# Kernel tuning notes

Measured on AMD Instinct MI355X. Metric: run time of the kernel, lower is better.

## Reference

```python
import jax, jax.numpy as jnp
import numpy as np

N_HEADS, N_LEVELS, N_POINTS = 8, 4, 4
D_MODEL, RNN, ENC, ATT_HID = 512, 512, 512, 512
D_HEAD = D_MODEL // N_HEADS  # att_feat_size = clip_context_dim / cap_nheads = 64
B = 1024
LEVEL_LENS = [1024, 512, 256, 128]
T_TOTAL = sum(LEVEL_LENS)


def setup_inputs() -> dict:
    key = jax.random.key(0)
    ks = jax.random.split(key, 24)
    s = 0.02  # weight init scale
    inp = {
        'xt': jax.random.normal(ks[0], (B, ENC), jnp.float32),
        'h0': jax.random.normal(ks[1], (2, B, RNN), jnp.float32),
        'c0': jax.random.normal(ks[2], (2, B, RNN), jnp.float32),
        'query': jax.random.normal(ks[3], (1, B, D_MODEL), jnp.float32),
        'reference_points': jax.random.uniform(ks[4], (1, B, N_LEVELS, 1), jnp.float32),
        'input_flatten': jax.random.normal(ks[5], (1, T_TOTAL, D_MODEL), jnp.float32),
        'input_spatial_shapes': jnp.asarray(LEVEL_LENS, jnp.int32),
        'input_level_start_index': jnp.asarray(np.cumsum([0] + LEVEL_LENS[:-1]), jnp.int32),
        'input_padding_mask': jnp.zeros((1, T_TOTAL), jnp.bool_),
        # MSDeformAttnCap params (query side sees cat(h, query) -> 2*D_MODEL)
        'W_value': jax.random.normal(ks[6], (D_MODEL, D_MODEL), jnp.float32) * s,
        'b_value': jnp.zeros((D_MODEL,), jnp.float32),
        'W_off': jax.random.normal(ks[7], (2 * D_MODEL, N_HEADS * N_LEVELS * N_POINTS), jnp.float32) * s,
        'b_off': jax.random.normal(ks[8], (N_HEADS * N_LEVELS * N_POINTS,), jnp.float32) * s,
        'W_attw': jax.random.normal(ks[9], (2 * D_MODEL, N_HEADS * N_LEVELS * N_POINTS), jnp.float32) * s,
        'b_attw': jnp.zeros((N_HEADS * N_LEVELS * N_POINTS,), jnp.float32),
        # additive SAT attention
        'W_ctx': jax.random.normal(ks[10], (D_HEAD, ATT_HID), jnp.float32) * s,
        'b_ctx': jnp.zeros((ATT_HID,), jnp.float32),
        'W_h2a': jax.random.normal(ks[11], (RNN, ATT_HID), jnp.float32) * s,
        'b_h2a': jnp.zeros((ATT_HID,), jnp.float32),
        'w_alpha': jax.random.normal(ks[12], (ATT_HID, 1), jnp.float32) * s,
        'b_alpha': jnp.zeros((1,), jnp.float32),
        # 2-layer LSTM, bias=False; input = ENC + 2*D_MODEL = 1536
        'Wih0': jax.random.normal(ks[13], (4 * RNN, ENC + 2 * D_MODEL), jnp.float32) * s,
        'Whh0': jax.random.normal(ks[14], (4 * RNN, RNN), jnp.float32) * s,
        'Wih1': jax.random.normal(ks[15], (4 * RNN, RNN), jnp.float32) * s,
        'Whh1': jax.random.normal(ks[16], (4 * RNN, RNN), jnp.float32) * s,
    }
    return inp


def _lstm_cell(x, h, c, Wih, Whh):
    g = x @ Wih.T + h @ Whh.T
    i, f, gg, o = jnp.split(g, 4, axis=-1)
    c2 = jax.nn.sigmoid(f) * c + jax.nn.sigmoid(i) * jnp.tanh(gg)
    h2 = jax.nn.sigmoid(o) * jnp.tanh(c2)
    return h2, c2


def reference(xt, h0, c0, query, reference_points, input_flatten,
              input_spatial_shapes, input_level_start_index, input_padding_mask,
              W_value, b_value, W_off, b_off, W_attw, b_attw,
              W_ctx, b_ctx, W_h2a, b_h2a, w_alpha, b_alpha,
              Wih0, Whh0, Wih1, Whh1):
    h_last = h0[-1]                                            # (B, RNN)
    jq = jnp.concatenate([h_last, query[0]], axis=-1)          # (B, 2D) joint query

    # ---- MSDeformAttnCap: value proj + 1D multi-level point sampling ----
    v = input_flatten[0] @ W_value + b_value                   # (T, D)
    v = jnp.where(input_padding_mask[0][:, None], 0.0, v)
    v = v.reshape(-1, N_HEADS, D_HEAD).transpose(1, 0, 2)     # (H, T, Dh)

    off = (jq @ W_off + b_off).reshape(B, N_HEADS, N_LEVELS, N_POINTS)
    aw = (jq @ W_attw + b_attw).reshape(B, N_HEADS, N_LEVELS * N_POINTS)
    aw = jax.nn.softmax(aw, axis=-1).reshape(B, N_HEADS, N_LEVELS, N_POINTS)

    Tf = input_spatial_shapes.astype(jnp.float32)              # (L,)
    ref = reference_points[0, :, :, 0]                          # (B, L) normalized centers
    loc = ref[:, None, :, None] + off / Tf[None, None, :, None]  # (B,H,L,P) in [0,1]

    # grid_sample(align_corners=False, zeros padding) linear interp along T
    x = loc * Tf[None, None, :, None] - 0.5
    x0 = jnp.floor(x)
    w1 = x - x0
    Ti = input_spatial_shapes[None, None, :, None]
    x0i = x0.astype(jnp.int32)
    valid0 = ((x0i >= 0) & (x0i < Ti)).astype(v.dtype)
    valid1 = ((x0i + 1 >= 0) & (x0i + 1 < Ti)).astype(v.dtype)
    start = input_level_start_index[None, None, :, None]
    i0 = jnp.clip(x0i, 0, Ti - 1) + start
    i1 = jnp.clip(x0i + 1, 0, Ti - 1) + start
    hids = jnp.arange(N_HEADS)[None, :, None, None]
    v0 = v[hids, i0]                                            # (B,H,L,P,Dh)
    v1 = v[hids, i1]
    samp = v0 * ((1.0 - w1) * valid0)[..., None] + v1 * (w1 * valid1)[..., None]
    # weighted sampled values, NOT summed over points (Cap variant)
    clip_feats = (samp * aw[..., None]).reshape(B, N_HEADS, N_LEVELS * N_POINTS, D_HEAD)

    # ---- additive SAT attention over the L*P sampled slots ----
    att_h = h_last @ W_h2a + b_h2a                              # (B, A)
    att = jnp.tanh(clip_feats @ W_ctx + b_ctx + att_h[:, None, None, :])  # (B,H,LP,A)
    dot = (att @ w_alpha)[..., 0] + b_alpha[0]                  # (B,H,LP)
    w = jax.nn.softmax(dot, axis=-1)
    att_res = jnp.einsum('bhp,bhpd->bhd', w, clip_feats).reshape(B, N_HEADS * D_HEAD)

    # ---- LSTM step (2 layers, bias=False, eval mode -> no dropout) ----
    x_in = jnp.concatenate([xt, att_res, query[0]], axis=-1)   # (B, ENC+2D)
    h1, c1 = _lstm_cell(x_in, h0[0], c0[0], Wih0, Whh0)
    h2, c2 = _lstm_cell(h1, h0[1], c0[1], Wih1, Whh1)
    h_new = jnp.stack([h1, h2])
    c_new = jnp.stack([c1, c2])
    return h2, h_new, c_new
```

## Files before the change

kernel.cpp:

```cpp
#include <hip/hip_runtime.h>
#include <math.h>


typedef __attribute__((ext_vector_type(8))) short          s16x8;
typedef __attribute__((ext_vector_type(8))) unsigned short u16x8;
typedef __attribute__((ext_vector_type(4))) float          f32x4;

#define LOG2E  1.4426950408889634f
#define LOG2E2 2.8853900817779268f

__device__ __forceinline__ float rcpf(float x) { return __builtin_amdgcn_rcpf(x); }
__device__ __forceinline__ float exp2f_fast(float x) { return __builtin_amdgcn_exp2f(x); }
__device__ __forceinline__ float sigf(float x) {
    return rcpf(1.0f + exp2f_fast(-x * LOG2E));
}
__device__ __forceinline__ float tanhf_fast(float x) {
    const float xc = fminf(fmaxf(x, -15.0f), 15.0f);
    const float e2 = exp2f_fast(xc * LOG2E2);
    return 1.0f - 2.0f * rcpf(e2 + 1.0f);
}
__device__ __forceinline__ unsigned short f2bf(float f) {
    unsigned u = __float_as_uint(f);
    u += 0x7FFF + ((u >> 16) & 1);
    return (unsigned short)(u >> 16);
}
__device__ __forceinline__ float bf2f(unsigned short h) {
    return __uint_as_float(((unsigned)h) << 16);
}
__device__ __forceinline__ void gld_lds16(const unsigned short* g, unsigned short* l) {
    __builtin_amdgcn_global_load_lds(
        (const __attribute__((address_space(1))) void*)g,
        (__attribute__((address_space(3))) void*)l, 16, 0, 0);
}

struct CvtJob { const float* src; unsigned short* dst; int sld, dld, cols, total, ilv; };
struct CvtJobs { CvtJob j[11]; };
__global__ __launch_bounds__(256) void cvt_bf16(CvtJobs cj) {
    const CvtJob jb = cj.j[blockIdx.y];
    const int i = (blockIdx.x * 256 + threadIdx.x) * 4;
    if (i >= jb.total) return;
    const int r = i / jb.cols, c = i - r * jb.cols;
    const int rd = jb.ilv ? (((r & 511) << 2) | (r >> 9)) : r;
    const float4 v4 = *(const float4*)&jb.src[(size_t)r * jb.sld + c];
    ushort4 o;
    o.x = f2bf(v4.x); o.y = f2bf(v4.y); o.z = f2bf(v4.z); o.w = f2bf(v4.w);
    *(ushort4*)&jb.dst[(size_t)rd * jb.dld + c] = o;
}

struct TJob { const float* src; unsigned short* dst; int N_, dld, K_, total; };
struct TJobs { TJob j[6]; };
__global__ __launch_bounds__(256) void tcvt_bf16(TJobs tj) {
    const TJob jb = tj.j[blockIdx.y];
    const int tilesN = jb.N_ >> 5, tilesK = jb.K_ >> 5;
    const int tile = blockIdx.x;
    if (tile >= tilesN * tilesK) return;
    const int tn0 = (tile % tilesN) << 5, tk0 = (tile / tilesN) << 5;
    __shared__ float lds[32][33];
    const int t = threadIdx.x;
    if (jb.src) {
#pragma unroll
        for (int q = 0; q < 4; ++q) {
            const int e = t + (q << 8);
            lds[e >> 5][e & 31] = jb.src[(size_t)(tk0 + (e >> 5)) * jb.N_ + tn0 + (e & 31)];
        }
        __syncthreads();
#pragma unroll
        for (int q = 0; q < 4; ++q) {
            const int e = t + (q << 8);
            const int n = e >> 5, k = e & 31;
            jb.dst[(size_t)(tn0 + n) * jb.dld + tk0 + k] = f2bf(lds[k][n]);
        }
    } else {
#pragma unroll
        for (int q = 0; q < 4; ++q) {
            const int e = t + (q << 8);
            jb.dst[(size_t)(tn0 + (e >> 5)) * jb.dld + tk0 + (e & 31)] = 0;
        }
    }
}

__global__ __launch_bounds__(768) void bias_cat3(const float* __restrict__ a,
                                                 const float* __restrict__ b,
                                                 const float* __restrict__ c,
                                                 float* __restrict__ dst) {
    const int t = threadIdx.x;
    dst[t] = (t < 128) ? a[t] : (t < 256 ? b[t - 128] : c[t - 256]);
}


#define STAGE_T(buf, k0) do { \
        gld_lds16(Ag1 + (k0), &As[buf][s1 * 8]); \
        gld_lds16(Ag2 + (k0), &As[buf][s2 * 8]); \
        gld_lds16(Bg1 + (k0), &Bs[buf][s1 * 8]); \
        gld_lds16(Bg2 + (k0), &Bs[buf][s2 * 8]); } while (0)

#define WAIT_INFL(t) do { \
        const int infl_ = nsteps - 1 - (t); \
        if (infl_ >= 2)      asm volatile("s_waitcnt vmcnt(8)" ::: "memory"); \
        else if (infl_ == 1) asm volatile("s_waitcnt vmcnt(4)" ::: "memory"); \
        else                 asm volatile("s_waitcnt vmcnt(0)" ::: "memory"); \
        __builtin_amdgcn_s_barrier(); } while (0)

__global__ __launch_bounds__(256) void sgemm(
    const unsigned short* __restrict__ A, int lda,
    const unsigned short* __restrict__ B, int ldb,
    const float* __restrict__ bias, float* __restrict__ C, int ldc, int K)
{
    __shared__ unsigned short As[4][64 * 64];
    __shared__ unsigned short Bs[4][64 * 64];

    const int tid = threadIdx.x;
    const int w = tid >> 6, lane = tid & 63;
    const int wr = w >> 1, wc = w & 1;
    const int lr = lane & 15, lg = lane >> 4;
    const int bm = blockIdx.y, bn = blockIdx.x;

    const int s1 = tid, s2 = tid + 256;
    const int r1 = s1 >> 3, c1 = ((s1 & 7) ^ (r1 & 7)) << 3;
    const int r2 = s2 >> 3, c2 = ((s2 & 7) ^ (r2 & 7)) << 3;
    const unsigned short* Ag1 = A + (size_t)(bm * 64 + r1) * lda + c1;
    const unsigned short* Ag2 = A + (size_t)(bm * 64 + r2) * lda + c2;
    const unsigned short* Bg1 = B + (size_t)(bn * 64 + r1) * ldb + c1;
    const unsigned short* Bg2 = B + (size_t)(bn * 64 + r2) * ldb + c2;

    f32x4 acc[2][2];
#pragma unroll
    for (int mt = 0; mt < 2; ++mt)
#pragma unroll
        for (int nt = 0; nt < 2; ++nt) acc[mt][nt] = (f32x4){0.f, 0.f, 0.f, 0.f};

    const int nsteps = K >> 6;
    STAGE_T(0, 0);
    if (nsteps > 1) STAGE_T(1, 64);
    if (nsteps > 2) STAGE_T(2, 128);

    for (int t = 0; t < nsteps; ++t) {
        WAIT_INFL(t);
        if (t + 3 < nsteps)
            STAGE_T((t + 3) & 3, (t + 3) << 6);
        const unsigned short* Ab = &As[t & 3][0];
        const unsigned short* Bb = &Bs[t & 3][0];
        s16x8 a[2][2], bfr[2][2];
#pragma unroll
        for (int mt = 0; mt < 2; ++mt) {
            const int ar = wr * 32 + mt * 16 + lr;
#pragma unroll
            for (int ks = 0; ks < 2; ++ks)
                a[mt][ks] = *(const s16x8*)&Ab[(ar * 8 + ((ks * 4 + lg) ^ (ar & 7))) * 8];
        }
#pragma unroll
        for (int nt = 0; nt < 2; ++nt) {
            const int br = wc * 32 + nt * 16 + lr;
#pragma unroll
            for (int ks = 0; ks < 2; ++ks)
                bfr[nt][ks] = *(const s16x8*)&Bb[(br * 8 + ((ks * 4 + lg) ^ (br & 7))) * 8];
        }
#pragma unroll
        for (int ks = 0; ks < 2; ++ks)
#pragma unroll
            for (int mt = 0; mt < 2; ++mt)
#pragma unroll
                for (int nt = 0; nt < 2; ++nt)
                    acc[mt][nt] = __builtin_amdgcn_mfma_f32_16x16x32_bf16(
                        a[mt][ks], bfr[nt][ks], acc[mt][nt], 0, 0, 0);
    }
#pragma unroll
    for (int nt = 0; nt < 2; ++nt) {
        const int col = bn * 64 + wc * 32 + nt * 16 + lr;
        const float bb = bias ? bias[col] : 0.0f;
#pragma unroll
        for (int mt = 0; mt < 2; ++mt) {
            const int rbase = bm * 64 + wr * 32 + mt * 16 + lg * 4;
#pragma unroll
            for (int r = 0; r < 4; ++r)
                C[(size_t)(rbase + r) * ldc + col] = acc[mt][nt][r] + bb;
        }
    }
}

__global__ __launch_bounds__(256) void sgemm_lstm(
    const unsigned short* __restrict__ A, int lda,
    const unsigned short* __restrict__ B, int ldb,
    const float* __restrict__ c_in,
    float* __restrict__ h_a, float* __restrict__ h_b,
    unsigned short* __restrict__ hbf, int hbf_ld,
    float* __restrict__ c_out, int K)
{
    __shared__ unsigned short As[4][64 * 64];
    __shared__ unsigned short Bs[4][64 * 64];

    const int tid = threadIdx.x;
    const int w = tid >> 6, lane = tid & 63;
    const int wr = w >> 1, wc = w & 1;
    const int lr = lane & 15, lg = lane >> 4;
    const int bm = blockIdx.y, bn = blockIdx.x;

    const int s1 = tid, s2 = tid + 256;
    const int r1 = s1 >> 3, c1 = ((s1 & 7) ^ (r1 & 7)) << 3;
    const int r2 = s2 >> 3, c2 = ((s2 & 7) ^ (r2 & 7)) << 3;
    const unsigned short* Ag1 = A + (size_t)(bm * 64 + r1) * lda + c1;
    const unsigned short* Ag2 = A + (size_t)(bm * 64 + r2) * lda + c2;
    const unsigned short* Bg1 = B + (size_t)(bn * 64 + r1) * ldb + c1;
    const unsigned short* Bg2 = B + (size_t)(bn * 64 + r2) * ldb + c2;

    f32x4 acc[2][2];
#pragma unroll
    for (int mt = 0; mt < 2; ++mt)
#pragma unroll
        for (int nt = 0; nt < 2; ++nt) acc[mt][nt] = (f32x4){0.f, 0.f, 0.f, 0.f};

    const int nsteps = K >> 6;
    STAGE_T(0, 0);
    if (nsteps > 1) STAGE_T(1, 64);
    if (nsteps > 2) STAGE_T(2, 128);

    for (int t = 0; t < nsteps; ++t) {
        WAIT_INFL(t);
        if (t + 3 < nsteps)
            STAGE_T((t + 3) & 3, (t + 3) << 6);
        const unsigned short* Ab = &As[t & 3][0];
        const unsigned short* Bb = &Bs[t & 3][0];
        s16x8 a[2][2], bfr[2][2];
#pragma unroll
        for (int mt = 0; mt < 2; ++mt) {
            const int ar = wr * 32 + mt * 16 + lr;
#pragma unroll
            for (int ks = 0; ks < 2; ++ks)
                a[mt][ks] = *(const s16x8*)&Ab[(ar * 8 + ((ks * 4 + lg) ^ (ar & 7))) * 8];
        }
#pragma unroll
        for (int nt = 0; nt < 2; ++nt) {
            const int br = wc * 32 + nt * 16 + lr;
#pragma unroll
            for (int ks = 0; ks < 2; ++ks)
                bfr[nt][ks] = *(const s16x8*)&Bb[(br * 8 + ((ks * 4 + lg) ^ (br & 7))) * 8];
        }
#pragma unroll
        for (int ks = 0; ks < 2; ++ks)
#pragma unroll
            for (int mt = 0; mt < 2; ++mt)
#pragma unroll
                for (int nt = 0; nt < 2; ++nt)
                    acc[mt][nt] = __builtin_amdgcn_mfma_f32_16x16x32_bf16(
                        a[mt][ks], bfr[nt][ks], acc[mt][nt], 0, 0, 0);
    }
    const int gte  = lane & 3;
    const int base = lane & ~3;
#pragma unroll
    for (int nt = 0; nt < 2; ++nt) {
        const int col = bn * 64 + wc * 32 + nt * 16 + lr;
        const int u = col >> 2;
#pragma unroll
        for (int mt = 0; mt < 2; ++mt) {
            const int rbase = bm * 64 + wr * 32 + mt * 16 + lg * 4;
#pragma unroll
            for (int r = 0; r < 4; ++r) {
                const float vv = acc[mt][nt][r];
                const float a  = (gte == 2) ? tanhf_fast(vv) : sigf(vv);
                const float ai = __shfl(a, base + 0);
                const float af = __shfl(a, base + 1);
                const float ag = __shfl(a, base + 2);
                const float ao = __shfl(a, base + 3);
                const int row = rbase + r;
                const float c  = c_in[(size_t)row * 512 + u];
                const float c2 = af * c + ai * ag;
                const float h2 = ao * tanhf_fast(c2);
                if (gte == 0)      c_out[(size_t)row * 512 + u] = c2;
                else if (gte == 1) h_a[(size_t)row * 512 + u] = h2;
                else if (gte == 2) { if (h_b) h_b[(size_t)row * 512 + u] = h2; }
                else if (hbf)      hbf[(size_t)row * hbf_ld + u] = f2bf(h2);
            }
        }
    }
}
#undef STAGE_T
#undef WAIT_INFL

__global__ __launch_bounds__(512, 2) void fused_att(
    const float* __restrict__ v,
    const float* __restrict__ obat,
    const float* __restrict__ refp,
    const int*   __restrict__ shapes,
    const int*   __restrict__ starts,
    const unsigned short* __restrict__ Wb,
    const float* __restrict__ bctx,
    const float* __restrict__ walpha,
    unsigned short* __restrict__ attdst)
{
    __shared__ unsigned short cf[128 * 64];
    __shared__ float ba[512];
    __shared__ float wal[512];
    __shared__ float awb[128];
    __shared__ float dsum[128];
    __shared__ float dots4[4][128];

    const int b   = blockIdx.x;
    const int tid = threadIdx.x;

    if (tid < 128) awb[tid] = obat[b * 768 + 128 + tid];
    __syncthreads();
    if (tid < 8) {
        float mx = -1e30f;
        for (int i = 0; i < 16; ++i) mx = fmaxf(mx, awb[tid * 16 + i]);
        float sum = 0.f;
        for (int i = 0; i < 16; ++i) { float e = exp2f_fast((awb[tid * 16 + i] - mx) * LOG2E); awb[tid * 16 + i] = e; sum += e; }
        float inv = rcpf(sum);
        for (int i = 0; i < 16; ++i) awb[tid * 16 + i] *= inv;
    }
    __syncthreads();

    ba[tid]  = bctx[tid] + obat[b * 768 + 256 + tid];
    wal[tid] = walpha[tid];
    {
        const int pg  = tid >> 2;
        const int sub = tid & 3;
        const int d0  = sub * 16;
        const int h   = pg >> 4;
        const int l   = (pg & 15) >> 2;
        const int Tlen = shapes[l];
        const int st   = starts[l];
        const float T  = (float)Tlen;
        const float refv = refp[b * 4 + l];
        const float offv = obat[b * 768 + pg];
        const float awv  = awb[pg];
        const float x   = (refv + offv * rcpf(T)) * T - 0.5f;
        const float x0f = floorf(x);
        const float w1  = x - x0f;
        const int   x0  = (int)x0f;
        const float w0s = (x0 >= 0 && x0 < Tlen) ? (1.0f - w1) : 0.0f;
        const float w1s = (x0 + 1 >= 0 && x0 + 1 < Tlen) ? w1 : 0.0f;
        const int i0 = (min(max(x0, 0), Tlen - 1) + st) * 512 + h * 64;
        const int i1 = (min(max(x0 + 1, 0), Tlen - 1) + st) * 512 + h * 64;
        u16x8 o0, o1;
#pragma unroll
        for (int q = 0; q < 4; ++q) {
            const float4 a  = *(const float4*)&v[i0 + d0 + q * 4];
            const float4 bq = *(const float4*)&v[i1 + d0 + q * 4];
            unsigned short e0 = f2bf((a.x * w0s + bq.x * w1s) * awv);
            unsigned short e1 = f2bf((a.y * w0s + bq.y * w1s) * awv);
            unsigned short e2 = f2bf((a.z * w0s + bq.z * w1s) * awv);
            unsigned short e3 = f2bf((a.w * w0s + bq.w * w1s) * awv);
            if (q == 0) { o0[0] = e0; o0[1] = e1; o0[2] = e2; o0[3] = e3; }
            if (q == 1) { o0[4] = e0; o0[5] = e1; o0[6] = e2; o0[7] = e3; }
            if (q == 2) { o1[0] = e0; o1[1] = e1; o1[2] = e2; o1[3] = e3; }
            if (q == 3) { o1[4] = e0; o1[5] = e1; o1[6] = e2; o1[7] = e3; }
        }
        const int c0 = (sub * 2)     ^ (pg & 7);
        const int c1 = (sub * 2 + 1) ^ (pg & 7);
        *(u16x8*)&cf[pg * 64 + c0 * 8] = o0;
        *(u16x8*)&cf[pg * 64 + c1 * 8] = o1;
    }
    __syncthreads();

    {
        const int w    = tid >> 6, lane = tid & 63;
        const int wm   = w >> 2, wn = w & 3;
        const int lr   = lane & 15, lg = lane >> 4;

        s16x8 afrag[4][2];
#pragma unroll
        for (int mt = 0; mt < 4; ++mt) {
            const int row = wm * 64 + mt * 16 + lr;
#pragma unroll
            for (int ks = 0; ks < 2; ++ks) {
                const int ch = (ks * 4 + lg) ^ (row & 7);
                afrag[mt][ks] = *(const s16x8*)&cf[row * 64 + ch * 8];
            }
        }
        f32x4 part[4];
#pragma unroll
        for (int mt = 0; mt < 4; ++mt) part[mt] = (f32x4){0.f, 0.f, 0.f, 0.f};

#pragma clang loop unroll(disable)
        for (int nt = 0; nt < 8; ++nt) {
            const int ct  = wn * 8 + nt;
            const int col = ct * 16 + lr;
            const s16x8 b0 = *(const s16x8*)&Wb[col * 64 + lg * 8];
            const s16x8 b1 = *(const s16x8*)&Wb[col * 64 + 32 + lg * 8];
            const float bav = ba[col], wav = wal[col];
#pragma unroll
            for (int mt = 0; mt < 4; ++mt) {
                f32x4 acc = {0.f, 0.f, 0.f, 0.f};
                acc = __builtin_amdgcn_mfma_f32_16x16x32_bf16(afrag[mt][0], b0, acc, 0, 0, 0);
                acc = __builtin_amdgcn_mfma_f32_16x16x32_bf16(afrag[mt][1], b1, acc, 0, 0, 0);
#pragma unroll
                for (int r = 0; r < 4; ++r)
                    part[mt][r] += tanhf_fast(acc[r] + bav) * wav;
            }
        }
#pragma unroll
        for (int mt = 0; mt < 4; ++mt) {
#pragma unroll
            for (int r = 0; r < 4; ++r) {
                float s = part[mt][r];
                s += __shfl_xor(s, 1); s += __shfl_xor(s, 2);
                s += __shfl_xor(s, 4); s += __shfl_xor(s, 8);
                if (lr == 0) dots4[wn][wm * 64 + mt * 16 + lg * 4 + r] = s;
            }
        }
    }
    __syncthreads();
    if (tid < 128)
        dsum[tid] = dots4[0][tid] + dots4[1][tid] + dots4[2][tid] + dots4[3][tid];
    __syncthreads();

    if (tid < 8) {
        float mx = -1e30f;
        for (int i = 0; i < 16; ++i) mx = fmaxf(mx, dsum[tid * 16 + i]);
        float sum = 0.f;
        for (int i = 0; i < 16; ++i) { float e = exp2f_fast((dsum[tid * 16 + i] - mx) * LOG2E); dsum[tid * 16 + i] = e; sum += e; }
        float inv = rcpf(sum);
        for (int i = 0; i < 16; ++i) dsum[tid * 16 + i] *= inv;
    }
    __syncthreads();

    {
        const int h = tid >> 6, d = tid & 63;
        const int ch = d >> 3, e = d & 7;
        float s = 0.f;
#pragma unroll
        for (int p = 0; p < 16; ++p) {
            const int row = h * 16 + p;
            s += dsum[h * 16 + p] * bf2f(cf[row * 64 + ((ch ^ (row & 7)) * 8) + e]);
        }
        attdst[(size_t)b * 2048 + tid] = f2bf(s);
    }
}

extern "C" void kernel_launch(void* const* d_in, const int* in_sizes, int n_in,
                              void* d_out, int out_size, void* d_ws, size_t ws_size,
                              hipStream_t stream) {
    const float* xt     = (const float*)d_in[0];
    const float* h0     = (const float*)d_in[1];
    const float* c0     = (const float*)d_in[2];
    const float* query  = (const float*)d_in[3];
    const float* refp   = (const float*)d_in[4];
    const float* inflat = (const float*)d_in[5];
    const int*   shapes = (const int*)d_in[6];
    const int*   starts = (const int*)d_in[7];
    const float* Wv     = (const float*)d_in[9];
    const float* bv     = (const float*)d_in[10];
    const float* Woff   = (const float*)d_in[11];
    const float* boff   = (const float*)d_in[12];
    const float* Wattw  = (const float*)d_in[13];
    const float* battw  = (const float*)d_in[14];
    const float* Wctx   = (const float*)d_in[15];
    const float* bctx   = (const float*)d_in[16];
    const float* Wh2a   = (const float*)d_in[17];
    const float* bh2a   = (const float*)d_in[18];
    const float* walpha = (const float*)d_in[19];
    const float* Wih0   = (const float*)d_in[21];
    const float* Whh0   = (const float*)d_in[22];
    const float* Wih1   = (const float*)d_in[23];
    const float* Whh1   = (const float*)d_in[24];

    float* out = (float*)d_out;
    float* ws  = (float*)d_ws;

    float*          v     = ws;
    float*          obat  = ws + 983040;
    unsigned short* Acat  = (unsigned short*)(ws + 1769472);
    unsigned short* Bcat0 = (unsigned short*)(ws + 2818048);
    unsigned short* Ainf  = (unsigned short*)(ws + 4915200);
    unsigned short* Wvt   = (unsigned short*)(ws + 5406720);
    unsigned short* Wcat  = (unsigned short*)(ws + 5537792);
    unsigned short* Ahq   = (unsigned short*)(ws + 5931008);
    unsigned short* Wb    = (unsigned short*)(ws + 6455296);
    float*          bcat  = ws + 6471680;
    unsigned short* Ag1   = (unsigned short*)(ws + 7012352);
    unsigned short* Bcat1 = (unsigned short*)(ws + 7536640);

    const float* h00    = h0;
    const float* h_last = h0 + 524288;
    float* h1  = out + 524288;
    float* c1  = out + 1572864;
    float* h2a = out;
    float* h2b = out + 1048576;
    float* c2  = out + 2097152;

    { CvtJobs cj;
      cj.j[0]  = { xt,     Acat,          512,  2048, 512,  524288,  0 };
      cj.j[1]  = { query,  Acat + 1024,   512,  2048, 512,  524288,  0 };
      cj.j[2]  = { h00,    Acat + 1536,   512,  2048, 512,  524288,  0 };
      cj.j[3]  = { h_last, Ahq,           512,  1024, 512,  524288,  0 };
      cj.j[4]  = { query,  Ahq + 512,     512,  1024, 512,  524288,  0 };
      cj.j[5]  = { h_last, Ag1 + 512,     512,  1024, 512,  524288,  0 };
      cj.j[6]  = { Wih0,   Bcat0,         1536, 2048, 1536, 3145728, 1 };
      cj.j[7]  = { Whh0,   Bcat0 + 1536,  512,  2048, 512,  1048576, 1 };
      cj.j[8]  = { Wih1,   Bcat1,         512,  1024, 512,  1048576, 1 };
      cj.j[9]  = { Whh1,   Bcat1 + 512,   512,  1024, 512,  1048576, 1 };
      cj.j[10] = { inflat, Ainf,          512,  512,  512,  983040,  0 };
      cvt_bf16<<<dim3(3072, 11), 256, 0, stream>>>(cj); }
    { TJobs tj;
      tj.j[0] = { Wv,      Wvt,                     512, 512,  512, 0 };
      tj.j[1] = { Woff,    Wcat,                    128, 1024, 1024, 0 };
      tj.j[2] = { Wattw,   Wcat + 128 * 1024,       128, 1024, 1024, 0 };
      tj.j[3] = { Wh2a,    Wcat + 256 * 1024,       512, 1024, 512, 0 };
      tj.j[4] = { Wctx,    Wb,                      512, 64,   64,  0 };
      tj.j[5] = { nullptr, Wcat + 256 * 1024 + 512, 512, 1024, 512, 0 };
      tcvt_bf16<<<dim3(256, 6), 256, 0, stream>>>(tj); }
    bias_cat3<<<1, 768, 0, stream>>>(boff, battw, bh2a, bcat);

    sgemm<<<dim3(8, 30), 256, 0, stream>>>(Ainf, 512, Wvt, 512, bv, v, 512, 512);
    sgemm<<<dim3(12, 16), 256, 0, stream>>>(Ahq, 1024, Wcat, 1024, bcat, obat, 768, 1024);

    fused_att<<<1024, 512, 0, stream>>>(v, obat, refp, shapes, starts,
                                        Wb, bctx, walpha, Acat + 512);

    sgemm_lstm<<<dim3(32, 16), 256, 0, stream>>>(Acat, 2048, Bcat0, 2048,
                                                 c0, h1, nullptr, Ag1, 1024, c1, 2048);
    sgemm_lstm<<<dim3(32, 16), 256, 0, stream>>>(Ag1, 1024, Bcat1, 1024,
                                                 c0 + 524288, h1 - 524288, h2b, nullptr, 0, c2, 1024);
}
```

Before: 120.6 us.

## Merge two independent GEMMs into one launch and split attention per head-half

The value projection GEMM and the query/offset GEMM are merged into a single grouped launch of 432 blocks, with each block picking its job from its block index. This removes one launch and lets the two small grids fill the GPU together. The fused attention kernel now uses two 256-thread blocks per batch row, each handling four heads, which halves per-block LDS and allows more blocks per CU. The cost is that each block recomputes the shared bias vector and reloads the Wb fragments.

```diff
diff --git a/kernel.cpp b/kernel.cpp
--- a/kernel.cpp
+++ b/kernel.cpp
@@ -101,27 +101,31 @@
         else                 asm volatile("s_waitcnt vmcnt(0)" ::: "memory"); \
         __builtin_amdgcn_s_barrier(); } while (0)
 
-__global__ __launch_bounds__(256) void sgemm(
-    const unsigned short* __restrict__ A, int lda,
-    const unsigned short* __restrict__ B, int ldb,
-    const float* __restrict__ bias, float* __restrict__ C, int ldc, int K)
-{
+struct GJob { const unsigned short* A; int lda; const unsigned short* B; int ldb;
+              const float* bias; float* C; int ldc; int K; int nbx; int count; };
+struct GJobs { GJob j[2]; };
+__global__ __launch_bounds__(256) void sgemm2(GJobs gj) {
     __shared__ unsigned short As[4][64 * 64];
     __shared__ unsigned short Bs[4][64 * 64];
+
+    int bid = blockIdx.x;
+    GJob jb = gj.j[0];
+    if (bid >= jb.count) { bid -= jb.count; jb = gj.j[1]; }
+    const int bn = bid % jb.nbx, bm = bid / jb.nbx;
+    const int lda = jb.lda, ldb = jb.ldb;
 
     const int tid = threadIdx.x;
     const int w = tid >> 6, lane = tid & 63;
     const int wr = w >> 1, wc = w & 1;
     const int lr = lane & 15, lg = lane >> 4;
-    const int bm = blockIdx.y, bn = blockIdx.x;
 
     const int s1 = tid, s2 = tid + 256;
     const int r1 = s1 >> 3, c1 = ((s1 & 7) ^ (r1 & 7)) << 3;
     const int r2 = s2 >> 3, c2 = ((s2 & 7) ^ (r2 & 7)) << 3;
-    const unsigned short* Ag1 = A + (size_t)(bm * 64 + r1) * lda + c1;
-    const unsigned short* Ag2 = A + (size_t)(bm * 64 + r2) * lda + c2;
-    const unsigned short* Bg1 = B + (size_t)(bn * 64 + r1) * ldb + c1;
-    const unsigned short* Bg2 = B + (size_t)(bn * 64 + r2) * ldb + c2;
+    const unsigned short* Ag1 = jb.A + (size_t)(bm * 64 + r1) * lda + c1;
+    const unsigned short* Ag2 = jb.A + (size_t)(bm * 64 + r2) * lda + c2;
+    const unsigned short* Bg1 = jb.B + (size_t)(bn * 64 + r1) * ldb + c1;
+    const unsigned short* Bg2 = jb.B + (size_t)(bn * 64 + r2) * ldb + c2;
 
     f32x4 acc[2][2];
 #pragma unroll
@@ -129,15 +133,14 @@
 #pragma unroll
         for (int nt = 0; nt < 2; ++nt) acc[mt][nt] = (f32x4){0.f, 0.f, 0.f, 0.f};
 
-    const int nsteps = K >> 6;
+    const int nsteps = jb.K >> 6;
     STAGE_T(0, 0);
     if (nsteps > 1) STAGE_T(1, 64);
     if (nsteps > 2) STAGE_T(2, 128);
 
     for (int t = 0; t < nsteps; ++t) {
         WAIT_INFL(t);
-        if (t + 3 < nsteps)
-            STAGE_T((t + 3) & 3, (t + 3) << 6);
+        if (t + 3 < nsteps) STAGE_T((t + 3) & 3, (t + 3) << 6);
         const unsigned short* Ab = &As[t & 3][0];
         const unsigned short* Bb = &Bs[t & 3][0];
         s16x8 a[2][2], bfr[2][2];
@@ -167,13 +170,13 @@
 #pragma unroll
     for (int nt = 0; nt < 2; ++nt) {
         const int col = bn * 64 + wc * 32 + nt * 16 + lr;
-        const float bb = bias ? bias[col] : 0.0f;
+        const float bb = jb.bias ? jb.bias[col] : 0.0f;
 #pragma unroll
         for (int mt = 0; mt < 2; ++mt) {
             const int rbase = bm * 64 + wr * 32 + mt * 16 + lg * 4;
 #pragma unroll
             for (int r = 0; r < 4; ++r)
-                C[(size_t)(rbase + r) * ldc + col] = acc[mt][nt][r] + bb;
+                jb.C[(size_t)(rbase + r) * jb.ldc + col] = acc[mt][nt][r] + bb;
         }
     }
 }
@@ -216,8 +219,7 @@
 
     for (int t = 0; t < nsteps; ++t) {
         WAIT_INFL(t);
-        if (t + 3 < nsteps)
-            STAGE_T((t + 3) & 3, (t + 3) << 6);
+        if (t + 3 < nsteps) STAGE_T((t + 3) & 3, (t + 3) << 6);
         const unsigned short* Ab = &As[t & 3][0];
         const unsigned short* Bb = &Bs[t & 3][0];
         s16x8 a[2][2], bfr[2][2];
@@ -276,7 +278,7 @@
 #undef STAGE_T
 #undef WAIT_INFL
 
-__global__ __launch_bounds__(512, 2) void fused_att(
+__global__ __launch_bounds__(256, 4) void fused_att(
     const float* __restrict__ v,
     const float* __restrict__ obat,
     const float* __restrict__ refp,
@@ -287,19 +289,20 @@
     const float* __restrict__ walpha,
     unsigned short* __restrict__ attdst)
 {
-    __shared__ unsigned short cf[128 * 64];
+    __shared__ unsigned short cf[64 * 64];
     __shared__ float ba[512];
     __shared__ float wal[512];
-    __shared__ float awb[128];
-    __shared__ float dsum[128];
-    __shared__ float dots4[4][128];
-
-    const int b   = blockIdx.x;
+    __shared__ float awb[64];
+    __shared__ float dsum[64];
+    __shared__ float dots4[4][64];
+
+    const int b   = blockIdx.x >> 1;
+    const int hh  = blockIdx.x & 1;
     const int tid = threadIdx.x;
 
-    if (tid < 128) awb[tid] = obat[b * 768 + 128 + tid];
+    if (tid < 64) awb[tid] = obat[b * 768 + 128 + hh * 64 + tid];
     __syncthreads();
-    if (tid < 8) {
+    if (tid < 4) {
         float mx = -1e30f;
         for (int i = 0; i < 16; ++i) mx = fmaxf(mx, awb[tid * 16 + i]);
         float sum = 0.f;
@@ -309,12 +312,15 @@
     }
     __syncthreads();
 
-    ba[tid]  = bctx[tid] + obat[b * 768 + 256 + tid];
-    wal[tid] = walpha[tid];
+    ba[tid]        = bctx[tid]       + obat[b * 768 + 256 + tid];
+    ba[tid + 256]  = bctx[tid + 256] + obat[b * 768 + 512 + tid];
+    wal[tid]       = walpha[tid];
+    wal[tid + 256] = walpha[tid + 256];
     {
-        const int pg  = tid >> 2;
+        const int pl  = tid >> 2;
         const int sub = tid & 3;
         const int d0  = sub * 16;
+        const int pg  = hh * 64 + pl;
         const int h   = pg >> 4;
         const int l   = (pg & 15) >> 2;
         const int Tlen = shapes[l];
@@ -322,7 +328,7 @@
         const float T  = (float)Tlen;
         const float refv = refp[b * 4 + l];
         const float offv = obat[b * 768 + pg];
-        const float awv  = awb[pg];
+        const float awv  = awb[pl];
         const float x   = (refv + offv * rcpf(T)) * T - 0.5f;
         const float x0f = floorf(x);
         const float w1  = x - x0f;
@@ -345,22 +351,21 @@
             if (q == 2) { o1[0] = e0; o1[1] = e1; o1[2] = e2; o1[3] = e3; }
             if (q == 3) { o1[4] = e0; o1[5] = e1; o1[6] = e2; o1[7] = e3; }
         }
-        const int c0 = (sub * 2)     ^ (pg & 7);
-        const int c1 = (sub * 2 + 1) ^ (pg & 7);
-        *(u16x8*)&cf[pg * 64 + c0 * 8] = o0;
-        *(u16x8*)&cf[pg * 64 + c1 * 8] = o1;
+        const int c0 = (sub * 2)     ^ (pl & 7);
+        const int c1 = (sub * 2 + 1) ^ (pl & 7);
+        *(u16x8*)&cf[pl * 64 + c0 * 8] = o0;
+        *(u16x8*)&cf[pl * 64 + c1 * 8] = o1;
     }
     __syncthreads();
 
     {
-        const int w    = tid >> 6, lane = tid & 63;
-        const int wm   = w >> 2, wn = w & 3;
+        const int wn   = tid >> 6, lane = tid & 63;
         const int lr   = lane & 15, lg = lane >> 4;
 
         s16x8 afrag[4][2];
 #pragma unroll
         for (int mt = 0; mt < 4; ++mt) {
-            const int row = wm * 64 + mt * 16 + lr;
+            const int row = mt * 16 + lr;
 #pragma unroll
             for (int ks = 0; ks < 2; ++ks) {
                 const int ch = (ks * 4 + lg) ^ (row & 7);
@@ -373,8 +378,7 @@
 
 #pragma clang loop unroll(disable)
         for (int nt = 0; nt < 8; ++nt) {
-            const int ct  = wn * 8 + nt;
-            const int col = ct * 16 + lr;
+            const int col = (wn * 8 + nt) * 16 + lr;
             const s16x8 b0 = *(const s16x8*)&Wb[col * 64 + lg * 8];
             const s16x8 b1 = *(const s16x8*)&Wb[col * 64 + 32 + lg * 8];
             const float bav = ba[col], wav = wal[col];
@@ -395,16 +399,16 @@
                 float s = part[mt][r];
                 s += __shfl_xor(s, 1); s += __shfl_xor(s, 2);
                 s += __shfl_xor(s, 4); s += __shfl_xor(s, 8);
-                if (lr == 0) dots4[wn][wm * 64 + mt * 16 + lg * 4 + r] = s;
+                if (lr == 0) dots4[wn][mt * 16 + lg * 4 + r] = s;
             }
         }
     }
     __syncthreads();
-    if (tid < 128)
+    if (tid < 64)
         dsum[tid] = dots4[0][tid] + dots4[1][tid] + dots4[2][tid] + dots4[3][tid];
     __syncthreads();
 
-    if (tid < 8) {
+    if (tid < 4) {
         float mx = -1e30f;
         for (int i = 0; i < 16; ++i) mx = fmaxf(mx, dsum[tid * 16 + i]);
         float sum = 0.f;
@@ -415,15 +419,15 @@
     __syncthreads();
 
     {
-        const int h = tid >> 6, d = tid & 63;
+        const int hl = tid >> 6, d = tid & 63;
         const int ch = d >> 3, e = d & 7;
         float s = 0.f;
 #pragma unroll
         for (int p = 0; p < 16; ++p) {
-            const int row = h * 16 + p;
-            s += dsum[h * 16 + p] * bf2f(cf[row * 64 + ((ch ^ (row & 7)) * 8) + e]);
-        }
-        attdst[(size_t)b * 2048 + tid] = f2bf(s);
+            const int row = hl * 16 + p;
+            s += dsum[hl * 16 + p] * bf2f(cf[row * 64 + ((ch ^ (row & 7)) * 8) + e]);
+        }
+        attdst[(size_t)b * 2048 + hh * 256 + tid] = f2bf(s);
     }
 }
 
@@ -501,10 +505,12 @@
       tcvt_bf16<<<dim3(256, 6), 256, 0, stream>>>(tj); }
     bias_cat3<<<1, 768, 0, stream>>>(boff, battw, bh2a, bcat);
 
-    sgemm<<<dim3(8, 30), 256, 0, stream>>>(Ainf, 512, Wvt, 512, bv, v, 512, 512);
-    sgemm<<<dim3(12, 16), 256, 0, stream>>>(Ahq, 1024, Wcat, 1024, bcat, obat, 768, 1024);
-
-    fused_att<<<1024, 512, 0, stream>>>(v, obat, refp, shapes, starts,
+    { GJobs gj;
+      gj.j[0] = { Ainf, 512,  Wvt,  512,  bv,   v,    512, 512,  8,  240 };
+      gj.j[1] = { Ahq,  1024, Wcat, 1024, bcat, obat, 768, 1024, 12, 192 };
+      sgemm2<<<432, 256, 0, stream>>>(gj); }
+
+    fused_att<<<2048, 256, 0, stream>>>(v, obat, refp, shapes, starts,
                                         Wb, bctx, walpha, Acat + 512);
 
     sgemm_lstm<<<dim3(32, 16), 256, 0, stream>>>(Acat, 2048, Bcat0, 2048,
```

Result: faster. 113.7 us (-5.7%).
